# Optimization experiments

Hardware: AMD Instinct MI355X
Metric: run time of the kernel (lower is better)

Reference implementation:

```python
import jax, jax.numpy as jnp
import numpy as np

N = 100000
E = 1000000
F_IN = 64
HID = 128
NCLS = 32
G = 1024
EPS = 1e-5


def setup_inputs() -> dict:
    key = jax.random.key(0)
    ks = jax.random.split(key, 6)
    x = jax.random.normal(ks[0], (N, F_IN), dtype=jnp.float32)
    edge_index = jax.random.randint(ks[1], (2, E), 0, N, dtype=jnp.int64)
    batch = jnp.sort(jax.random.randint(ks[2], (N,), 0, G, dtype=jnp.int64))
    # parameters (init per _init_weights: uniform(-0.01,0.01) linears, BN w=0.1 b=0)
    W_gcn = jax.random.uniform(ks[3], (F_IN, HID), minval=-0.01, maxval=0.01, dtype=jnp.float32)
    b_gcn = jnp.zeros((HID,), jnp.float32)
    bn1_w = jnp.full((HID,), 0.1, jnp.float32)
    bn1_b = jnp.zeros((HID,), jnp.float32)
    W_out = jax.random.uniform(ks[4], (HID, NCLS), minval=-0.01, maxval=0.01, dtype=jnp.float32)
    b_out = jnp.zeros((NCLS,), jnp.float32)
    bn2_w = jnp.full((NCLS,), 0.1, jnp.float32)
    bn2_b = jnp.zeros((NCLS,), jnp.float32)
    return {"x": x, "edge_index": edge_index, "batch": batch,
            "W_gcn": W_gcn, "b_gcn": b_gcn, "bn1_w": bn1_w, "bn1_b": bn1_b,
            "W_out": W_out, "b_out": b_out, "bn2_w": bn2_w, "bn2_b": bn2_b}


def _batchnorm(h, w, b):
    # training-mode BN: biased batch statistics over dim 0
    mu = jnp.mean(h, axis=0)
    var = jnp.var(h, axis=0)
    return (h - mu) * jax.lax.rsqrt(var + EPS) * w + b


def reference(x, edge_index, batch, W_gcn, b_gcn, bn1_w, bn1_b, W_out, b_out, bn2_w, bn2_b):
    # --- GCNConv: add self loops, symmetric norm, transform, aggregate ---
    loop = jnp.arange(N, dtype=edge_index.dtype)
    src = jnp.concatenate([edge_index[0], loop])  # [E+N]
    dst = jnp.concatenate([edge_index[1], loop])
    deg = jax.ops.segment_sum(jnp.ones_like(dst, dtype=x.dtype), dst, num_segments=N)
    dinv = jax.lax.rsqrt(deg)  # deg >= 1 thanks to self loops
    coef = dinv[src] * dinv[dst]  # [E+N]
    h = x @ W_gcn  # [N, HID] transform before gather (as PyG)
    msg = h[src] * coef[:, None]  # [E+N, HID] gathered messages
    h = jax.ops.segment_sum(msg, dst, num_segments=N) + b_gcn
    # --- BN + ReLU (dropout is identity in eval) ---
    h = jax.nn.relu(_batchnorm(h, bn1_w, bn1_b))
    # --- global_mean_pool over graphs ---
    sums = jax.ops.segment_sum(h, batch, num_segments=G)  # [G, HID]
    cnt = jax.ops.segment_sum(jnp.ones((N,), h.dtype), batch, num_segments=G)
    pooled = sums / jnp.maximum(cnt, 1.0)[:, None]
    # --- head: Linear + BN ---
    out = pooled @ W_out + b_out
    return _batchnorm(out, bn2_w, bn2_b)
```

## Files before the change

kernel.cpp:

```cpp
#include <hip/hip_runtime.h>
#include <hip/hip_fp16.h>

constexpr int N    = 100000;
constexpr int E    = 1000000;
constexpr int FIN  = 64;
constexpr int HID  = 128;
constexpr int NCLS = 32;
constexpr int G    = 1024;
constexpr float EPS = 1e-5f;

constexpr int NTILE = (N + 127) / 128;

constexpr int NBUCK = 196;
constexpr int NPB   = 512;
constexpr int EPB   = 2048;
constexpr int CAP   = 6144;
constexpr int BIN_GRID = (E + EPB - 1) / EPB;

typedef _Float16 half2v __attribute__((ext_vector_type(2)));

__device__ inline float fdot2f(__half2 a, __half2 b, float c) {
#if __has_builtin(__builtin_amdgcn_fdot2)
  return __builtin_amdgcn_fdot2(*(half2v*)&a, *(half2v*)&b, c, false);
#else
  float2 fa = __half22float2(a), fb = __half22float2(b);
  return c + fa.x * fb.x + fa.y * fb.y;
#endif
}

__global__ __launch_bounds__(256) void k_bin(const int* __restrict__ src,
                                             const int* __restrict__ dst,
                                             int* __restrict__ bucketCursor,
                                             unsigned* __restrict__ bucketBuf) {
  __shared__ int bcnt[NBUCK];
  __shared__ int incl[256];
  __shared__ int bdelta[NBUCK];
  __shared__ int lcur[NBUCK];
  __shared__ unsigned staged[EPB];
  int tid = threadIdx.x;
  int e0 = blockIdx.x * EPB;
  int cnt = E - e0 < EPB ? E - e0 : EPB;
  for (int i = tid; i < NBUCK; i += 256) bcnt[i] = 0;
  __syncthreads();
  for (int i = tid; i < cnt; i += 256) {
    atomicAdd(&bcnt[dst[e0 + i] >> 9], 1);
  }
  __syncthreads();
  incl[tid] = (tid < NBUCK) ? bcnt[tid] : 0;
  __syncthreads();
  for (int off = 1; off < 256; off <<= 1) {
    int t = (tid >= off) ? incl[tid - off] : 0;
    __syncthreads();
    incl[tid] += t;
    __syncthreads();
  }
  if (tid < NBUCK) {
    int excl = incl[tid] - bcnt[tid];
    int base = bcnt[tid] ? atomicAdd(&bucketCursor[tid], bcnt[tid]) : 0;
    bdelta[tid] = base - excl;
    lcur[tid]   = excl;
  }
  __syncthreads();
  for (int i = tid; i < cnt; i += 256) {
    int s = src[e0 + i], d = dst[e0 + i];
    int pos = atomicAdd(&lcur[d >> 9], 1);
    staged[pos] = ((unsigned)(d & 511) << 17) | (unsigned)s;
  }
  __syncthreads();
  for (int i = tid; i < cnt; i += 256) {
    unsigned p = staged[i];
    int lo = 0, hi = NBUCK - 1;
    while (lo < hi) { int m = (lo + hi) >> 1; if (incl[m] > i) hi = m; else lo = m + 1; }
    bucketBuf[(long long)lo * CAP + bdelta[lo] + i] = p;
  }
}

__global__ __launch_bounds__(512) void k_build(const int* __restrict__ bucketLen,
                                               const unsigned* __restrict__ bucketBuf,
                                               int* __restrict__ offsets,
                                               float* __restrict__ dinv,
                                               int* __restrict__ srclist) {
  __shared__ int cnt[NPB];
  __shared__ int part[512];
  __shared__ int pre[256];
  __shared__ int sh_bbase;
  int b = blockIdx.x, tid = threadIdx.x;
  int n0 = b << 9;
  int nn = (N - n0 < NPB) ? (N - n0) : NPB;
  int len = bucketLen[b];
  cnt[tid] = 0;
  if (tid < 256) pre[tid] = (tid < NBUCK) ? bucketLen[tid] : 0;
  __syncthreads();
  for (int off = 1; off < 256; off <<= 1) {
    int t = 0;
    if (tid < 256 && tid >= off) t = pre[tid - off];
    __syncthreads();
    if (tid < 256) pre[tid] += t;
    __syncthreads();
  }
  if (tid == b) sh_bbase = pre[b] - len;
  __syncthreads();
  const unsigned* buf = bucketBuf + (long long)b * CAP;
  for (int i = tid; i < len; i += 512)
    atomicAdd(&cnt[buf[i] >> 17], 1);
  __syncthreads();
  int v = cnt[tid];
  part[tid] = v;
  __syncthreads();
  for (int off = 1; off < 512; off <<= 1) {
    int t = (tid >= off) ? part[tid - off] : 0;
    __syncthreads();
    part[tid] += t;
    __syncthreads();
  }
  int o = sh_bbase + part[tid] - v;
  __syncthreads();
  cnt[tid] = o;
  if (tid < nn) {
    offsets[n0 + tid] = o;
    dinv[n0 + tid] = rsqrtf((float)v + 1.0f);
  }
  if (b == NBUCK - 1 && tid == 511) offsets[N] = sh_bbase + part[511];
  __syncthreads();
  for (int i = tid; i < len; i += 512) {
    unsigned p = buf[i];
    int pos = atomicAdd(&cnt[p >> 17], 1);
    srclist[pos] = (int)(p & 0x1FFFFu);
  }
}

__global__ void k_scale(const float4* __restrict__ x4, const float* __restrict__ dinv,
                        float2* __restrict__ y2) {
  int i = blockIdx.x * blockDim.x + threadIdx.x;
  if (i >= N * 16) return;
  int node = i >> 4;
  float c = dinv[node];
  float4 v = x4[i];
  union { float2 f; __half2 h[2]; } u;
  u.h[0] = __float22half2_rn(make_float2(v.x * c, v.y * c));
  u.h[1] = __float22half2_rn(make_float2(v.z * c, v.w * c));
  y2[i] = u.f;
}

__global__ void k_wprep(const float* __restrict__ W, __half2* __restrict__ w2g,
                        int* __restrict__ bucketCursor, float* __restrict__ sums) {
  int idx = blockIdx.x * blockDim.x + threadIdx.x;
  if (blockIdx.x == 0) bucketCursor[threadIdx.x] = 0;
  if (blockIdx.x == 1 && threadIdx.x < 64) {
    float* p = sums + threadIdx.x;
    p[0] = 0.f; p[64] = 0.f; p[128] = 0.f; p[192] = 0.f; p[256] = 0.f;
  }
  if (idx >= 32 * 128) return;
  int kp = idx >> 7, col = idx & 127;
  w2g[idx] = __floats2half2_rn(W[(2 * kp) * 128 + col], W[(2 * kp + 1) * 128 + col]);
}

__global__ __launch_bounds__(256) void k_gather(const int* __restrict__ offsets,
                                                const int* __restrict__ srclist,
                                                const float* __restrict__ dinv,
                                                const float2* __restrict__ y2,
                                                float2* __restrict__ aggh) {
  int node = blockIdx.x * 16 + (threadIdx.x >> 4);
  int lane = threadIdx.x & 15;
  if (node >= N) return;
  int start = offsets[node], end = offsets[node + 1];
  float cd = dinv[node];

  union { float2 f; __half2 h[2]; } u;
  float4 a0, a1, a2, a3;
  u.f = y2[node * 16 + lane];
  {
    float2 f01 = __half22float2(u.h[0]);
    float2 f23 = __half22float2(u.h[1]);
    a0 = make_float4(f01.x, f01.y, f23.x, f23.y);
  }
  a1 = make_float4(0.f, 0.f, 0.f, 0.f);
  a2 = a1; a3 = a1;

  int i = start;
  for (; i + 3 < end; i += 4) {
    int s0 = srclist[i], s1 = srclist[i + 1], s2 = srclist[i + 2], s3 = srclist[i + 3];
    union { float2 f; __half2 h[2]; } u0, u1, u2, u3;
    u0.f = y2[(long long)s0 * 16 + lane];
    u1.f = y2[(long long)s1 * 16 + lane];
    u2.f = y2[(long long)s2 * 16 + lane];
    u3.f = y2[(long long)s3 * 16 + lane];
    float2 p, q;
    p = __half22float2(u0.h[0]); q = __half22float2(u0.h[1]);
    a0.x += p.x; a0.y += p.y; a0.z += q.x; a0.w += q.y;
    p = __half22float2(u1.h[0]); q = __half22float2(u1.h[1]);
    a1.x += p.x; a1.y += p.y; a1.z += q.x; a1.w += q.y;
    p = __half22float2(u2.h[0]); q = __half22float2(u2.h[1]);
    a2.x += p.x; a2.y += p.y; a2.z += q.x; a2.w += q.y;
    p = __half22float2(u3.h[0]); q = __half22float2(u3.h[1]);
    a3.x += p.x; a3.y += p.y; a3.z += q.x; a3.w += q.y;
  }
  for (; i < end; ++i) {
    int s = srclist[i];
    u.f = y2[(long long)s * 16 + lane];
    float2 p = __half22float2(u.h[0]);
    float2 q = __half22float2(u.h[1]);
    a0.x += p.x; a0.y += p.y; a0.z += q.x; a0.w += q.y;
  }
  float4 acc;
  acc.x = ((a0.x + a1.x) + (a2.x + a3.x)) * cd;
  acc.y = ((a0.y + a1.y) + (a2.y + a3.y)) * cd;
  acc.z = ((a0.z + a1.z) + (a2.z + a3.z)) * cd;
  acc.w = ((a0.w + a1.w) + (a2.w + a3.w)) * cd;
  union { float2 f; __half2 h[2]; } o;
  o.h[0] = __floats2half2_rn(acc.x, acc.y);
  o.h[1] = __floats2half2_rn(acc.z, acc.w);
  aggh[node * 16 + lane] = o.f;
}

__global__ __launch_bounds__(256) void k_gemm2h(const __half2* __restrict__ aggh2,
                                                const __half2* __restrict__ w2g,
                                                const float* __restrict__ b,
                                                __half2* __restrict__ h2,
                                                float* __restrict__ sums) {
  __shared__ __half2 Wl[32 * 128];
  __shared__ __half2 rowT[32 * 128];
  int tid  = threadIdx.x;
  int row0 = blockIdx.x * 128;
  {
    const float4* srcv = (const float4*)w2g;
    float4* dstv = (float4*)Wl;
    for (int i = tid; i < 1024; i += 256) dstv[i] = srcv[i];
  }
  {
    int half = tid >> 7;
    int r = tid & 127;
    int grow = row0 + r;
#pragma unroll
    for (int c = 0; c < 4; ++c) {
      int kp0 = half * 16 + c * 4;
      float4 v = make_float4(0.f, 0.f, 0.f, 0.f);
      if (grow < N) v = *(const float4*)&aggh2[(long long)grow * 32 + kp0];
      __half2* pv = (__half2*)&v;
      rowT[(kp0 + 0) * 128 + r] = pv[0];
      rowT[(kp0 + 1) * 128 + r] = pv[1];
      rowT[(kp0 + 2) * 128 + r] = pv[2];
      rowT[(kp0 + 3) * 128 + r] = pv[3];
    }
  }
  __syncthreads();

  int rt = tid >> 4, ct = tid & 15;
  float acc[8][8];
#pragma unroll
  for (int m = 0; m < 8; ++m)
#pragma unroll
    for (int j = 0; j < 8; ++j) acc[m][j] = 0.f;

#pragma unroll 2
  for (int kp = 0; kp < 32; ++kp) {
    float4 wv0 = *(const float4*)&Wl[kp * 128 + ct * 8];
    float4 wv1 = *(const float4*)&Wl[kp * 128 + ct * 8 + 4];
    float4 rv0 = *(const float4*)&rowT[kp * 128 + rt * 8];
    float4 rv1 = *(const float4*)&rowT[kp * 128 + rt * 8 + 4];
    __half2 wv[8], rv[8];
    *(float4*)&wv[0] = wv0; *(float4*)&wv[4] = wv1;
    *(float4*)&rv[0] = rv0; *(float4*)&rv[4] = rv1;
#pragma unroll
    for (int m = 0; m < 8; ++m)
#pragma unroll
      for (int j = 0; j < 8; ++j) acc[m][j] = fdot2f(rv[m], wv[j], acc[m][j]);
  }

  int cbase = ct * 8;
  float4 b0 = *(const float4*)&b[cbase];
  float4 b1 = *(const float4*)&b[cbase + 4];
  float bias[8] = {b0.x, b0.y, b0.z, b0.w, b1.x, b1.y, b1.z, b1.w};
  float s[8], s2[8];
#pragma unroll
  for (int j = 0; j < 8; ++j) { s[j] = 0.f; s2[j] = 0.f; }
#pragma unroll
  for (int m = 0; m < 8; ++m) {
    int grow = row0 + rt * 8 + m;
    if (grow < N) {
      float hv[8];
#pragma unroll
      for (int j = 0; j < 8; ++j) {
        hv[j] = acc[m][j] + bias[j];
        s[j] += hv[j];
        s2[j] += hv[j] * hv[j];
      }
      union { float4 f; __half2 h[4]; } o;
      o.h[0] = __floats2half2_rn(hv[0], hv[1]);
      o.h[1] = __floats2half2_rn(hv[2], hv[3]);
      o.h[2] = __floats2half2_rn(hv[4], hv[5]);
      o.h[3] = __floats2half2_rn(hv[6], hv[7]);
      *(float4*)&h2[(long long)grow * 64 + ct * 4] = o.f;
    }
  }
  __syncthreads();
  float* red = (float*)Wl;
#pragma unroll
  for (int j = 0; j < 8; ++j) {
    red[rt * 256 + cbase + j]       = s[j];
    red[rt * 256 + 128 + cbase + j] = s2[j];
  }
  __syncthreads();
  float tot = 0.f;
#pragma unroll 4
  for (int r = 0; r < 16; ++r) tot += red[r * 256 + tid];
  atomicAdd(&sums[tid], tot);
}

__global__ __launch_bounds__(128) void k_bn1_final(const float* __restrict__ sums,
                                                   const float* __restrict__ w,
                                                   const float* __restrict__ bb,
                                                   float* __restrict__ ss) {
  int tid = threadIdx.x;
  float mu  = sums[tid] * (1.0f / N);
  float var = sums[tid + 128] * (1.0f / N) - mu * mu;
  float rs  = rsqrtf(var + EPS);
  float sc  = rs * w[tid];
  ss[tid]       = sc;
  ss[tid + 128] = bb[tid] - mu * sc;
}

__global__ __launch_bounds__(256) void k_pool(const __half2* __restrict__ h2,
                                              const float* __restrict__ ss,
                                              const int* __restrict__ batch,
                                              float* __restrict__ pooled) {
  int g = blockIdx.x;
  int lo = 0, hi = N;
  while (lo < hi) { int m = (lo + hi) >> 1; if (batch[m] < g) lo = m + 1; else hi = m; }
  int lo2 = lo, hi2 = N;
  while (lo2 < hi2) { int m = (lo2 + hi2) >> 1; if (batch[m] < g + 1) lo2 = m + 1; else hi2 = m; }
  int start = lo, end = lo2;
  int tid = threadIdx.x;
  int cp = tid & 63, rp = tid >> 6;
  float sc0 = ss[2 * cp], sc1 = ss[2 * cp + 1];
  float sh0 = ss[2 * cp + 128], sh1 = ss[2 * cp + 129];
  float s0 = 0.f, s1 = 0.f;
  for (int r = start + rp; r < end; r += 4) {
    float2 f = __half22float2(h2[(long long)r * 64 + cp]);
    s0 += fmaxf(f.x * sc0 + sh0, 0.f);
    s1 += fmaxf(f.y * sc1 + sh1, 0.f);
  }
  __shared__ float red0[256], red1[256];
  red0[tid] = s0; red1[tid] = s1;
  __syncthreads();
  if (tid < 64) {
#pragma unroll
    for (int q = 1; q < 4; ++q) { s0 += red0[tid + q * 64]; s1 += red1[tid + q * 64]; }
    float cnt = fmaxf((float)(end - start), 1.0f);
    float2 o = make_float2(s0 / cnt, s1 / cnt);
    *(float2*)&pooled[g * 128 + 2 * tid] = o;
  }
}

__global__ __launch_bounds__(256) void k_head(const float* __restrict__ pooled,
                                              const float* __restrict__ W,
                                              const float* __restrict__ b,
                                              float* __restrict__ outpre,
                                              float* __restrict__ sums2) {
  int idx = blockIdx.x * 256 + threadIdx.x;
  int g = idx >> 5, c = idx & 31;
  float acc = b[c];
  const float* pr = pooled + g * 128;
#pragma unroll
  for (int k = 0; k < 128; ++k) acc += pr[k] * W[k * 32 + c];
  outpre[idx] = acc;
  __shared__ float red[256], red2[256];
  int tid = threadIdx.x;
  red[tid] = acc; red2[tid] = acc * acc;
  __syncthreads();
  for (int off = 128; off >= 32; off >>= 1) {
    if (tid < off) { red[tid] += red[tid + off]; red2[tid] += red2[tid + off]; }
    __syncthreads();
  }
  if (tid < 32) {
    atomicAdd(&sums2[tid], red[tid]);
    atomicAdd(&sums2[tid + 32], red2[tid]);
  }
}

__global__ void k_bn2f(const float* __restrict__ sums2, const float* __restrict__ w,
                       const float* __restrict__ b, float* __restrict__ ss2) {
  int c = threadIdx.x;
  float mu  = sums2[c] * (1.0f / G);
  float var = sums2[c + 32] * (1.0f / G) - mu * mu;
  float rs  = rsqrtf(var + EPS);
  float sc  = rs * w[c];
  ss2[c]      = sc;
  ss2[c + 32] = b[c] - mu * sc;
}

__global__ void k_bn2apply(const float* __restrict__ outpre, const float* __restrict__ ss2,
                           float* __restrict__ out) {
  int idx = blockIdx.x * 256 + threadIdx.x;
  int c = idx & 31;
  out[idx] = outpre[idx] * ss2[c] + ss2[c + 32];
}

extern "C" void kernel_launch(void* const* d_in, const int* in_sizes, int n_in,
                              void* d_out, int out_size, void* d_ws, size_t ws_size,
                              hipStream_t stream) {
  const float* x   = (const float*)d_in[0];
  const int* ei    = (const int*)d_in[1];
  const int* batch = (const int*)d_in[2];
  const float* Wg  = (const float*)d_in[3];
  const float* bg  = (const float*)d_in[4];
  const float* w1  = (const float*)d_in[5];
  const float* b1  = (const float*)d_in[6];
  const float* Wo  = (const float*)d_in[7];
  const float* bo  = (const float*)d_in[8];
  const float* w2  = (const float*)d_in[9];
  const float* b2  = (const float*)d_in[10];

  float* ws     = (float*)d_ws;
  float* dinv   = ws;
  float* y2f    = dinv + 100352;
  float* aggh_f = y2f + 3200000;
  float* h2f    = aggh_f + 1600512;
  float* ss     = h2f + 6400000;
  float* sums   = ss + 256;
  float* sums2  = sums + 256;
  float* ss2    = sums2 + 64;
  float* pooled = ss2 + 64;
  float* outpre = pooled + G * 128;
  int* offsets  = (int*)(outpre + G * 32);
  int* srclist  = offsets + 100416;
  int* bucketCursor = srclist + E;
  __half2* w2g  = (__half2*)(bucketCursor + 256);
  unsigned* bucketBuf = (unsigned*)((float*)w2g + 4096);

  const int* src = ei;
  const int* dst = ei + E;

  k_wprep<<<16, 256, 0, stream>>>(Wg, w2g, bucketCursor, sums);
  k_bin<<<BIN_GRID, 256, 0, stream>>>(src, dst, bucketCursor, bucketBuf);
  k_build<<<NBUCK, 512, 0, stream>>>(bucketCursor, bucketBuf, offsets, dinv, srclist);
  k_scale<<<(N * 16 + 255) / 256, 256, 0, stream>>>((const float4*)x, dinv, (float2*)y2f);
  k_gather<<<(N + 15) / 16, 256, 0, stream>>>(offsets, srclist, dinv, (const float2*)y2f,
                                              (float2*)aggh_f);
  k_gemm2h<<<NTILE, 256, 0, stream>>>((const __half2*)aggh_f, w2g, bg,
                                      (__half2*)h2f, sums);
  k_bn1_final<<<1, 128, 0, stream>>>(sums, w1, b1, ss);
  k_pool<<<G, 256, 0, stream>>>((const __half2*)h2f, ss, batch, pooled);
  k_head<<<128, 256, 0, stream>>>(pooled, Wo, bo, outpre, sums2);
  k_bn2f<<<1, 32, 0, stream>>>(sums2, w2, b2, ss2);
  k_bn2apply<<<128, 256, 0, stream>>>(outpre, ss2, (float*)d_out);
}
```

Measured before the change: 217.6 us.

## Fuse scale into build, fold BN finalizers into consumers, widen gather unroll

Merges the x-scaling pass into the CSR build kernel using per-block shared dinv, and folds the two single-block BN finalize kernels into the pool and bn2-apply kernels, each recomputing the scale/shift per block. The gather loop is unrolled to 8 outstanding loads per iteration. Together these remove three kernel launches and add more memory-level parallelism to the gather. In exchange, the scale work now runs on only 196 blocks and the BN parameters are recomputed redundantly in every block.

```diff
diff --git a/kernel.cpp b/kernel.cpp
--- a/kernel.cpp
+++ b/kernel.cpp
@@ -79,10 +79,13 @@
                                                const unsigned* __restrict__ bucketBuf,
                                                int* __restrict__ offsets,
                                                float* __restrict__ dinv,
-                                               int* __restrict__ srclist) {
+                                               int* __restrict__ srclist,
+                                               const float4* __restrict__ x4,
+                                               float2* __restrict__ y2) {
   __shared__ int cnt[NPB];
   __shared__ int part[512];
   __shared__ int pre[256];
+  __shared__ float sdinv[NPB];
   __shared__ int sh_bbase;
   int b = blockIdx.x, tid = threadIdx.x;
   int n0 = b << 9;
@@ -114,11 +117,13 @@
     __syncthreads();
   }
   int o = sh_bbase + part[tid] - v;
+  float dv = rsqrtf((float)v + 1.0f);
+  sdinv[tid] = dv;
   __syncthreads();
   cnt[tid] = o;
   if (tid < nn) {
     offsets[n0 + tid] = o;
-    dinv[n0 + tid] = rsqrtf((float)v + 1.0f);
+    dinv[n0 + tid] = dv;
   }
   if (b == NBUCK - 1 && tid == 511) offsets[N] = sh_bbase + part[511];
   __syncthreads();
@@ -127,19 +132,17 @@
     int pos = atomicAdd(&cnt[p >> 17], 1);
     srclist[pos] = (int)(p & 0x1FFFFu);
   }
-}
-
-__global__ void k_scale(const float4* __restrict__ x4, const float* __restrict__ dinv,
-                        float2* __restrict__ y2) {
-  int i = blockIdx.x * blockDim.x + threadIdx.x;
-  if (i >= N * 16) return;
-  int node = i >> 4;
-  float c = dinv[node];
-  float4 v = x4[i];
-  union { float2 f; __half2 h[2]; } u;
-  u.h[0] = __float22half2_rn(make_float2(v.x * c, v.y * c));
-  u.h[1] = __float22half2_rn(make_float2(v.z * c, v.w * c));
-  y2[i] = u.f;
+  const float4* xr = x4 + (long long)n0 * 16;
+  float2* yr = y2 + (long long)n0 * 16;
+  int tot = nn * 16;
+  for (int i = tid; i < tot; i += 512) {
+    float c = sdinv[i >> 4];
+    float4 val = xr[i];
+    union { float2 f; __half2 h[2]; } u;
+    u.h[0] = __float22half2_rn(make_float2(val.x * c, val.y * c));
+    u.h[1] = __float22half2_rn(make_float2(val.z * c, val.w * c));
+    yr[i] = u.f;
+  }
 }
 
 __global__ void k_wprep(const float* __restrict__ W, __half2* __restrict__ w2g,
@@ -167,50 +170,46 @@
   float cd = dinv[node];
 
   union { float2 f; __half2 h[2]; } u;
-  float4 a0, a1, a2, a3;
-  u.f = y2[node * 16 + lane];
+  float4 a[4];
+  u.f = y2[(long long)node * 16 + lane];
   {
-    float2 f01 = __half22float2(u.h[0]);
-    float2 f23 = __half22float2(u.h[1]);
-    a0 = make_float4(f01.x, f01.y, f23.x, f23.y);
-  }
-  a1 = make_float4(0.f, 0.f, 0.f, 0.f);
-  a2 = a1; a3 = a1;
+    float2 p = __half22float2(u.h[0]), q = __half22float2(u.h[1]);
+    a[0] = make_float4(p.x, p.y, q.x, q.y);
+  }
+  a[1] = make_float4(0.f, 0.f, 0.f, 0.f);
+  a[2] = a[1]; a[3] = a[1];
 
   int i = start;
-  for (; i + 3 < end; i += 4) {
-    int s0 = srclist[i], s1 = srclist[i + 1], s2 = srclist[i + 2], s3 = srclist[i + 3];
-    union { float2 f; __half2 h[2]; } u0, u1, u2, u3;
-    u0.f = y2[(long long)s0 * 16 + lane];
-    u1.f = y2[(long long)s1 * 16 + lane];
-    u2.f = y2[(long long)s2 * 16 + lane];
-    u3.f = y2[(long long)s3 * 16 + lane];
-    float2 p, q;
-    p = __half22float2(u0.h[0]); q = __half22float2(u0.h[1]);
-    a0.x += p.x; a0.y += p.y; a0.z += q.x; a0.w += q.y;
-    p = __half22float2(u1.h[0]); q = __half22float2(u1.h[1]);
-    a1.x += p.x; a1.y += p.y; a1.z += q.x; a1.w += q.y;
-    p = __half22float2(u2.h[0]); q = __half22float2(u2.h[1]);
-    a2.x += p.x; a2.y += p.y; a2.z += q.x; a2.w += q.y;
-    p = __half22float2(u3.h[0]); q = __half22float2(u3.h[1]);
-    a3.x += p.x; a3.y += p.y; a3.z += q.x; a3.w += q.y;
+  for (; i + 7 < end; i += 8) {
+    int sdx[8];
+#pragma unroll
+    for (int k = 0; k < 8; ++k) sdx[k] = srclist[i + k];
+    float2 vv[8];
+#pragma unroll
+    for (int k = 0; k < 8; ++k) vv[k] = y2[(long long)sdx[k] * 16 + lane];
+#pragma unroll
+    for (int k = 0; k < 8; ++k) {
+      union { float2 f; __half2 h[2]; } w;
+      w.f = vv[k];
+      float2 p = __half22float2(w.h[0]), q = __half22float2(w.h[1]);
+      a[k & 3].x += p.x; a[k & 3].y += p.y; a[k & 3].z += q.x; a[k & 3].w += q.y;
+    }
   }
   for (; i < end; ++i) {
     int s = srclist[i];
     u.f = y2[(long long)s * 16 + lane];
-    float2 p = __half22float2(u.h[0]);
-    float2 q = __half22float2(u.h[1]);
-    a0.x += p.x; a0.y += p.y; a0.z += q.x; a0.w += q.y;
+    float2 p = __half22float2(u.h[0]), q = __half22float2(u.h[1]);
+    a[0].x += p.x; a[0].y += p.y; a[0].z += q.x; a[0].w += q.y;
   }
   float4 acc;
-  acc.x = ((a0.x + a1.x) + (a2.x + a3.x)) * cd;
-  acc.y = ((a0.y + a1.y) + (a2.y + a3.y)) * cd;
-  acc.z = ((a0.z + a1.z) + (a2.z + a3.z)) * cd;
-  acc.w = ((a0.w + a1.w) + (a2.w + a3.w)) * cd;
+  acc.x = ((a[0].x + a[1].x) + (a[2].x + a[3].x)) * cd;
+  acc.y = ((a[0].y + a[1].y) + (a[2].y + a[3].y)) * cd;
+  acc.z = ((a[0].z + a[1].z) + (a[2].z + a[3].z)) * cd;
+  acc.w = ((a[0].w + a[1].w) + (a[2].w + a[3].w)) * cd;
   union { float2 f; __half2 h[2]; } o;
   o.h[0] = __floats2half2_rn(acc.x, acc.y);
   o.h[1] = __floats2half2_rn(acc.z, acc.w);
-  aggh[node * 16 + lane] = o.f;
+  aggh[(long long)node * 16 + lane] = o.f;
 }
 
 __global__ __launch_bounds__(256) void k_gemm2h(const __half2* __restrict__ aggh2,
@@ -307,33 +306,32 @@
   atomicAdd(&sums[tid], tot);
 }
 
-__global__ __launch_bounds__(128) void k_bn1_final(const float* __restrict__ sums,
-                                                   const float* __restrict__ w,
-                                                   const float* __restrict__ bb,
-                                                   float* __restrict__ ss) {
-  int tid = threadIdx.x;
-  float mu  = sums[tid] * (1.0f / N);
-  float var = sums[tid + 128] * (1.0f / N) - mu * mu;
-  float rs  = rsqrtf(var + EPS);
-  float sc  = rs * w[tid];
-  ss[tid]       = sc;
-  ss[tid + 128] = bb[tid] - mu * sc;
-}
-
 __global__ __launch_bounds__(256) void k_pool(const __half2* __restrict__ h2,
-                                              const float* __restrict__ ss,
+                                              const float* __restrict__ sums,
+                                              const float* __restrict__ w1,
+                                              const float* __restrict__ b1,
                                               const int* __restrict__ batch,
                                               float* __restrict__ pooled) {
+  __shared__ float sss[256];
+  int tid = threadIdx.x;
+  if (tid < 128) {
+    float mu  = sums[tid] * (1.0f / N);
+    float var = sums[tid + 128] * (1.0f / N) - mu * mu;
+    float rs  = rsqrtf(var + EPS);
+    float sc  = rs * w1[tid];
+    sss[tid]       = sc;
+    sss[tid + 128] = b1[tid] - mu * sc;
+  }
   int g = blockIdx.x;
   int lo = 0, hi = N;
   while (lo < hi) { int m = (lo + hi) >> 1; if (batch[m] < g) lo = m + 1; else hi = m; }
   int lo2 = lo, hi2 = N;
   while (lo2 < hi2) { int m = (lo2 + hi2) >> 1; if (batch[m] < g + 1) lo2 = m + 1; else hi2 = m; }
   int start = lo, end = lo2;
-  int tid = threadIdx.x;
+  __syncthreads();
   int cp = tid & 63, rp = tid >> 6;
-  float sc0 = ss[2 * cp], sc1 = ss[2 * cp + 1];
-  float sh0 = ss[2 * cp + 128], sh1 = ss[2 * cp + 129];
+  float sc0 = sss[2 * cp], sc1 = sss[2 * cp + 1];
+  float sh0 = sss[2 * cp + 128], sh1 = sss[2 * cp + 129];
   float s0 = 0.f, s1 = 0.f;
   for (int r = start + rp; r < end; r += 4) {
     float2 f = __half22float2(h2[(long long)r * 64 + cp]);
@@ -378,22 +376,25 @@
   }
 }
 
-__global__ void k_bn2f(const float* __restrict__ sums2, const float* __restrict__ w,
-                       const float* __restrict__ b, float* __restrict__ ss2) {
-  int c = threadIdx.x;
-  float mu  = sums2[c] * (1.0f / G);
-  float var = sums2[c + 32] * (1.0f / G) - mu * mu;
-  float rs  = rsqrtf(var + EPS);
-  float sc  = rs * w[c];
-  ss2[c]      = sc;
-  ss2[c + 32] = b[c] - mu * sc;
-}
-
-__global__ void k_bn2apply(const float* __restrict__ outpre, const float* __restrict__ ss2,
-                           float* __restrict__ out) {
-  int idx = blockIdx.x * 256 + threadIdx.x;
+__global__ __launch_bounds__(256) void k_bn2apply(const float* __restrict__ outpre,
+                                                  const float* __restrict__ sums2,
+                                                  const float* __restrict__ w2,
+                                                  const float* __restrict__ b2,
+                                                  float* __restrict__ out) {
+  __shared__ float s2l[64];
+  int tid = threadIdx.x;
+  if (tid < 32) {
+    float mu  = sums2[tid] * (1.0f / G);
+    float var = sums2[tid + 32] * (1.0f / G) - mu * mu;
+    float rs  = rsqrtf(var + EPS);
+    float sc  = rs * w2[tid];
+    s2l[tid]      = sc;
+    s2l[tid + 32] = b2[tid] - mu * sc;
+  }
+  __syncthreads();
+  int idx = blockIdx.x * 256 + tid;
   int c = idx & 31;
-  out[idx] = outpre[idx] * ss2[c] + ss2[c + 32];
+  out[idx] = outpre[idx] * s2l[c] + s2l[c + 32];
 }
 
 extern "C" void kernel_launch(void* const* d_in, const int* in_sizes, int n_in,
@@ -416,11 +417,9 @@
   float* y2f    = dinv + 100352;
   float* aggh_f = y2f + 3200000;
   float* h2f    = aggh_f + 1600512;
-  float* ss     = h2f + 6400000;
-  float* sums   = ss + 256;
+  float* sums   = h2f + 6400000;
   float* sums2  = sums + 256;
-  float* ss2    = sums2 + 64;
-  float* pooled = ss2 + 64;
+  float* pooled = sums2 + 64;
   float* outpre = pooled + G * 128;
   int* offsets  = (int*)(outpre + G * 32);
   int* srclist  = offsets + 100416;
@@ -433,15 +432,13 @@
 
   k_wprep<<<16, 256, 0, stream>>>(Wg, w2g, bucketCursor, sums);
   k_bin<<<BIN_GRID, 256, 0, stream>>>(src, dst, bucketCursor, bucketBuf);
-  k_build<<<NBUCK, 512, 0, stream>>>(bucketCursor, bucketBuf, offsets, dinv, srclist);
-  k_scale<<<(N * 16 + 255) / 256, 256, 0, stream>>>((const float4*)x, dinv, (float2*)y2f);
+  k_build<<<NBUCK, 512, 0, stream>>>(bucketCursor, bucketBuf, offsets, dinv, srclist,
+                                     (const float4*)x, (float2*)y2f);
   k_gather<<<(N + 15) / 16, 256, 0, stream>>>(offsets, srclist, dinv, (const float2*)y2f,
                                               (float2*)aggh_f);
   k_gemm2h<<<NTILE, 256, 0, stream>>>((const __half2*)aggh_f, w2g, bg,
                                       (__half2*)h2f, sums);
-  k_bn1_final<<<1, 128, 0, stream>>>(sums, w1, b1, ss);
-  k_pool<<<G, 256, 0, stream>>>((const __half2*)h2f, ss, batch, pooled);
+  k_pool<<<G, 256, 0, stream>>>((const __half2*)h2f, sums, w1, b1, batch, pooled);
   k_head<<<128, 256, 0, stream>>>(pooled, Wo, bo, outpre, sums2);
-  k_bn2f<<<1, 32, 0, stream>>>(sums2, w2, b2, ss2);
-  k_bn2apply<<<128, 256, 0, stream>>>(outpre, ss2, (float*)d_out);
-}
+  k_bn2apply<<<128, 256, 0, stream>>>(outpre, sums2, w2, b2, (float*)d_out);
+}
```

Measured after the change: 218.8 us. No clear change (+0.6%).
